# Kernel tuning notes

Measured on AMD Instinct MI355X. Metric: run time of the kernel, lower is better.

The kernel has to match this reference:

```python
import jax, jax.numpy as jnp
import numpy as np

D = 512
H = 8
HD = D // H
EPS = 1e-5
NEG_INF = -1e30


def _ln(x, g, b):
    mu = jnp.mean(x, axis=-1, keepdims=True)
    var = jnp.mean(jnp.square(x - mu), axis=-1, keepdims=True)
    return (x - mu) * jax.lax.rsqrt(var + EPS) * g + b


def setup_inputs() -> dict:
    key = jax.random.key(0)
    ks = jax.random.split(key, 8)
    V, M, S = 128, 128, 514  # seq includes 2 head tokens (cls+dist)
    inp = {
        "video_embeds": jax.random.normal(ks[0], (V, D), jnp.float32),
        "music_features": jax.random.normal(ks[1], (M, S, D), jnp.float32),
        "music_masks": jnp.ones((M, S - 2), jnp.int32),
    }
    wk = jax.random.split(ks[2], 5)
    for name, k in zip(["Wq", "Wk", "Wv", "Wo", "Wl"], wk):
        inp[name] = jax.random.normal(k, (D, D), jnp.float32) * 0.02
    for name in ["bq", "bk", "bv", "bo", "bl"]:
        inp[name] = jnp.zeros((D,), jnp.float32)
    for name in ["g1", "g2", "g3"]:
        inp[name] = jnp.ones((D,), jnp.float32)
    for name in ["b1", "b2", "b3"]:
        inp[name] = jnp.zeros((D,), jnp.float32)
    return inp


def reference(video_embeds, music_features, music_masks,
              Wq, bq, Wk, bk, Wv, bv, Wo, bo, Wl, bl,
              g1, b1, g2, b2, g3, b3):
    # drop cls + dist tokens
    mf = music_features[:, 2:, :]  # (M, f, D)
    ve = _ln(video_embeds, g1, b1)  # (V, D)
    mf = _ln(mf, g1, b1)
    V = ve.shape[0]
    M, f, _ = mf.shape

    q = (ve @ Wq.T + bq).reshape(V, H, HD).transpose(1, 0, 2)        # (H, V, hd)
    k = (mf @ Wk.T + bk).reshape(M, f, H, HD).transpose(0, 2, 1, 3)  # (M, H, f, hd)
    v = (mf @ Wv.T + bv).reshape(M, f, H, HD).transpose(0, 2, 1, 3)  # (M, H, f, hd)

    logits = jnp.einsum('hvd,mhfd->vmhf', q, k) / np.sqrt(HD).astype(np.float32)
    mask = music_masks[None, :, None, :]  # (1, M, 1, f)
    logits = jnp.where(mask == 0, NEG_INF, logits)
    w = jax.nn.softmax(logits, axis=-1)
    attn = jnp.einsum('vmhf,mhfd->vmhd', w, v).reshape(V, M, D)
    attn = attn @ Wo.T + bo

    attn = _ln(attn, g2, b2)
    out = attn + (attn @ Wl.T + bl)  # dropout = identity in eval
    return _ln(out, g3, b3)
```

## Files before the change

### kernel.cpp

```cpp
#include <hip/hip_runtime.h>
#include <hip/hip_bf16.h>

typedef unsigned int uint;
typedef unsigned short ushort;
typedef __bf16 bf16;
typedef bf16 bf16x8 __attribute__((ext_vector_type(8)));
typedef float f32x4 __attribute__((ext_vector_type(4)));
typedef ushort ushort4v __attribute__((ext_vector_type(4)));

__device__ __forceinline__ float bf2f(ushort u) {
  union { uint u; float f; } v; v.u = ((uint)u) << 16; return v.f;
}
__device__ __forceinline__ ushort f2bf(float f) {
  union { float f; uint u; } v; v.f = f;
  uint u = v.u;
  uint r = (u + 0x7fffu + ((u >> 16) & 1u)) >> 16;
  return (ushort)r;
}

__device__ __forceinline__ void gl2lds16(const void* g, void* l) {
  __builtin_amdgcn_global_load_lds(
      (const __attribute__((address_space(1))) void*)g,
      (__attribute__((address_space(3))) void*)l, 16, 0, 0);
}

__device__ __forceinline__ void ln_rows(
    int mode, int nrows, int blk, int nblk, int tid,
    const void* __restrict__ srcA, const void* __restrict__ srcB,
    const float* __restrict__ g, const float* __restrict__ b,
    void* __restrict__ dst)
{
  const int l = tid & 63;
  const int nw = nblk * 4;
  for (int row = blk * 4 + (tid >> 6); row < nrows; row += nw) {
    float x[8];
    if (mode <= 1) {
      const float* s;
      if (mode == 0) {
        s = (const float*)srcA + (size_t)row * 512;
      } else {
        int mm = row >> 9, fi = row & 511;
        s = (const float*)srcA + ((size_t)mm * 514 + 2 + fi) * 512;
      }
      float4 a0 = *(const float4*)(s + l * 4);
      float4 a1 = *(const float4*)(s + 256 + l * 4);
      x[0] = a0.x; x[1] = a0.y; x[2] = a0.z; x[3] = a0.w;
      x[4] = a1.x; x[5] = a1.y; x[6] = a1.z; x[7] = a1.w;
    } else if (mode == 2) {
      const ushort* s = (const ushort*)srcA + (size_t)row * 512;
      uint4 u = *(const uint4*)(s + l * 8);
      x[0] = bf2f((ushort)u.x); x[1] = bf2f((ushort)(u.x >> 16));
      x[2] = bf2f((ushort)u.y); x[3] = bf2f((ushort)(u.y >> 16));
      x[4] = bf2f((ushort)u.z); x[5] = bf2f((ushort)(u.z >> 16));
      x[6] = bf2f((ushort)u.w); x[7] = bf2f((ushort)(u.w >> 16));
    } else {
      const ushort* sa = (const ushort*)srcA + (size_t)row * 512;
      const ushort* sb = (const ushort*)srcB + (size_t)row * 512;
      uint4 ua = *(const uint4*)(sa + l * 8);
      uint4 ub = *(const uint4*)(sb + l * 8);
      x[0] = bf2f((ushort)ua.x) + bf2f((ushort)ub.x);
      x[1] = bf2f((ushort)(ua.x >> 16)) + bf2f((ushort)(ub.x >> 16));
      x[2] = bf2f((ushort)ua.y) + bf2f((ushort)ub.y);
      x[3] = bf2f((ushort)(ua.y >> 16)) + bf2f((ushort)(ub.y >> 16));
      x[4] = bf2f((ushort)ua.z) + bf2f((ushort)ub.z);
      x[5] = bf2f((ushort)(ua.z >> 16)) + bf2f((ushort)(ub.z >> 16));
      x[6] = bf2f((ushort)ua.w) + bf2f((ushort)ub.w);
      x[7] = bf2f((ushort)(ua.w >> 16)) + bf2f((ushort)(ub.w >> 16));
    }
    float sum = 0.f, sq = 0.f;
    #pragma unroll
    for (int j = 0; j < 8; ++j) { sum += x[j]; sq += x[j] * x[j]; }
    #pragma unroll
    for (int o = 1; o < 64; o <<= 1) {
      sum += __shfl_xor(sum, o);
      sq  += __shfl_xor(sq, o);
    }
    const float inv = 1.f / 512.f;
    float mu = sum * inv;
    float var = sq * inv - mu * mu;
    float rstd = rsqrtf(var + 1e-5f);

    float gv[8], bv[8];
    if (mode <= 1) {
      float4 g0 = *(const float4*)(g + l * 4);
      float4 g1 = *(const float4*)(g + 256 + l * 4);
      float4 b0 = *(const float4*)(b + l * 4);
      float4 b1 = *(const float4*)(b + 256 + l * 4);
      gv[0] = g0.x; gv[1] = g0.y; gv[2] = g0.z; gv[3] = g0.w;
      gv[4] = g1.x; gv[5] = g1.y; gv[6] = g1.z; gv[7] = g1.w;
      bv[0] = b0.x; bv[1] = b0.y; bv[2] = b0.z; bv[3] = b0.w;
      bv[4] = b1.x; bv[5] = b1.y; bv[6] = b1.z; bv[7] = b1.w;
    } else {
      float4 g0 = *(const float4*)(g + l * 8);
      float4 g1 = *(const float4*)(g + l * 8 + 4);
      float4 b0 = *(const float4*)(b + l * 8);
      float4 b1 = *(const float4*)(b + l * 8 + 4);
      gv[0] = g0.x; gv[1] = g0.y; gv[2] = g0.z; gv[3] = g0.w;
      gv[4] = g1.x; gv[5] = g1.y; gv[6] = g1.z; gv[7] = g1.w;
      bv[0] = b0.x; bv[1] = b0.y; bv[2] = b0.z; bv[3] = b0.w;
      bv[4] = b1.x; bv[5] = b1.y; bv[6] = b1.z; bv[7] = b1.w;
    }
    float y[8];
    #pragma unroll
    for (int j = 0; j < 8; ++j) y[j] = (x[j] - mu) * rstd * gv[j] + bv[j];

    if (mode <= 1) {
      ushort* d = (ushort*)dst + (size_t)row * 512;
      ushort4v p0, p1;
      #pragma unroll
      for (int j = 0; j < 4; ++j) { p0[j] = f2bf(y[j]); p1[j] = f2bf(y[4 + j]); }
      *(ushort4v*)(d + l * 4) = p0;
      *(ushort4v*)(d + 256 + l * 4) = p1;
    } else if (mode == 2) {
      ushort* d = (ushort*)dst + (size_t)row * 512;
      uint4 o;
      o.x = (uint)f2bf(y[0]) | ((uint)f2bf(y[1]) << 16);
      o.y = (uint)f2bf(y[2]) | ((uint)f2bf(y[3]) << 16);
      o.z = (uint)f2bf(y[4]) | ((uint)f2bf(y[5]) << 16);
      o.w = (uint)f2bf(y[6]) | ((uint)f2bf(y[7]) << 16);
      *(uint4*)(d + l * 8) = o;
    } else {
      float* d = (float*)dst + (size_t)row * 512;
      float4 o0, o1;
      o0.x = y[0]; o0.y = y[1]; o0.z = y[2]; o0.w = y[3];
      o1.x = y[4]; o1.y = y[5]; o1.z = y[6]; o1.w = y[7];
      *(float4*)(d + l * 8) = o0;
      *(float4*)(d + l * 8 + 4) = o1;
    }
  }
}

__global__ __launch_bounds__(256) void ln512v(
    int mode, int nrows,
    const void* __restrict__ srcA, const void* __restrict__ srcB,
    const float* __restrict__ g, const float* __restrict__ b,
    void* __restrict__ dst)
{
  ln_rows(mode, nrows, blockIdx.x, gridDim.x, threadIdx.x, srcA, srcB, g, b, dst);
}

struct PreArgs {
  const float* s0; const float* s1; const float* s2; const float* s3; const float* s4;
  ushort* d0; ushort* d1; ushort* d2; ushort* d3; ushort* d4;
  const float* video; const float* music;
  const float* g1; const float* b1;
  ushort* veln; ushort* mfln;
};
__global__ __launch_bounds__(256) void preamble(PreArgs a) {
  int bb = blockIdx.x;
  if (bb < 640) {
    int t = bb * 256 + threadIdx.x;
    int which = t >> 15;
    int e = (t & 32767) * 8;
    const float* s = which == 0 ? a.s0 : which == 1 ? a.s1 : which == 2 ? a.s2 : which == 3 ? a.s3 : a.s4;
    ushort*      d = which == 0 ? a.d0 : which == 1 ? a.d1 : which == 2 ? a.d2 : which == 3 ? a.d3 : a.d4;
    float4 v0 = *(const float4*)(s + e);
    float4 v1 = *(const float4*)(s + e + 4);
    uint4 o;
    o.x = (uint)f2bf(v0.x) | ((uint)f2bf(v0.y) << 16);
    o.y = (uint)f2bf(v0.z) | ((uint)f2bf(v0.w) << 16);
    o.z = (uint)f2bf(v1.x) | ((uint)f2bf(v1.y) << 16);
    o.w = (uint)f2bf(v1.z) | ((uint)f2bf(v1.w) << 16);
    *(uint4*)(d + e) = o;
  } else if (bb < 672) {
    ln_rows(0, 128, bb - 640, 32, threadIdx.x, a.video, nullptr, a.g1, a.b1, a.veln);
  } else {
    ln_rows(1, 65536, bb - 672, 2048, threadIdx.x, a.music, nullptr, a.g1, a.b1, a.mfln);
  }
}

__global__ __launch_bounds__(256) void gemm_t3(
    const ushort* __restrict__ A, const ushort* __restrict__ W,
    const float* __restrict__ bias, ushort* __restrict__ C,
    float scale, int vt_mode)
{
  __shared__ __align__(16) ushort As[2][128 * 64];
  __shared__ __align__(16) ushort Bs[2][128 * 64];
  const int tid = threadIdx.x;
  const int w = tid >> 6, l = tid & 63;
  const int lg = l >> 4, lr = l & 15;
  const int wr = w >> 1, wc = w & 1;

  int nwg = gridDim.x * gridDim.y;
  int bid = blockIdx.y * gridDim.x + blockIdx.x;
  if ((nwg & 7) == 0) bid = (bid & 7) * (nwg >> 3) + (bid >> 3);
  const int bx = bid % gridDim.x, by = bid / gridDim.x;
  const int row0 = by * 128, col0 = bx * 128;

  f32x4 acc[4][4];
  #pragma unroll
  for (int i = 0; i < 4; i++)
    #pragma unroll
    for (int j = 0; j < 4; j++) { f32x4 z = {0.f,0.f,0.f,0.f}; acc[i][j] = z; }

  size_t asrc[4], wsrc[4]; int ldst[4];
  #pragma unroll
  for (int c2 = 0; c2 < 4; ++c2) {
    int c = c2 * 256 + tid;
    int r = c >> 3, j = c & 7;
    int koff = (j ^ (r & 7)) * 8;
    asrc[c2] = (size_t)(row0 + r) * 512 + koff;
    wsrc[c2] = (size_t)(col0 + r) * 512 + koff;
    ldst[c2] = (c2 * 256 + w * 64) * 8;
  }

  auto stage = [&](int pb, int kk) {
    #pragma unroll
    for (int c2 = 0; c2 < 4; ++c2) {
      gl2lds16(A + asrc[c2] + kk * 64, &As[pb][ldst[c2]]);
      gl2lds16(W + wsrc[c2] + kk * 64, &Bs[pb][ldst[c2]]);
    }
  };
  auto compute = [&](int pb) {
    #pragma unroll
    for (int ks = 0; ks < 2; ++ks) {
      bf16x8 af[4], bfr[4];
      #pragma unroll
      for (int mi = 0; mi < 4; ++mi) {
        int r = wr * 64 + mi * 16 + lr;
        af[mi] = *(const bf16x8*)(&As[pb][r * 64 + ((ks * 32 + lg * 8) ^ ((r & 7) * 8))]);
      }
      #pragma unroll
      for (int ni = 0; ni < 4; ++ni) {
        int r = wc * 64 + ni * 16 + lr;
        bfr[ni] = *(const bf16x8*)(&Bs[pb][r * 64 + ((ks * 32 + lg * 8) ^ ((r & 7) * 8))]);
      }
      #pragma unroll
      for (int mi = 0; mi < 4; ++mi)
        #pragma unroll
        for (int ni = 0; ni < 4; ++ni)
          acc[mi][ni] = __builtin_amdgcn_mfma_f32_16x16x32_bf16(af[mi], bfr[ni], acc[mi][ni], 0, 0, 0);
    }
  };

  stage(0, 0);
  __syncthreads();
  int cur = 0;
  #pragma unroll
  for (int kk = 0; kk < 7; ++kk) {
    stage(cur ^ 1, kk + 1);
    compute(cur);
    __syncthreads();
    cur ^= 1;
  }
  compute(cur);

  #pragma unroll
  for (int ni = 0; ni < 4; ++ni) {
    int cg = col0 + wc * 64 + ni * 16 + lr;
    float bc = bias[cg];
    #pragma unroll
    for (int mi = 0; mi < 4; ++mi) {
      int rg0 = row0 + wr * 64 + mi * 16 + lg * 4;
      if (!vt_mode) {
        #pragma unroll
        for (int e = 0; e < 4; ++e) {
          float v = (acc[mi][ni][e] + bc) * scale;
          C[(size_t)(rg0 + e) * 512 + cg] = f2bf(v);
        }
      } else {
        int m = rg0 >> 9, fi = rg0 & 511;
        ushort4v pk;
        #pragma unroll
        for (int e = 0; e < 4; ++e) pk[e] = f2bf((acc[mi][ni][e] + bc) * scale);
        *(ushort4v*)(C + (size_t)(m * 512 + cg) * 512 + fi) = pk;
      }
    }
  }
}

__global__ __launch_bounds__(256) void attn_kernel(
    const ushort* __restrict__ q, const ushort* __restrict__ k,
    const ushort* __restrict__ vt, const int* __restrict__ masks,
    ushort* __restrict__ attn)
{
  __shared__ __align__(16) ushort Qs[128 * 64];
  __shared__ __align__(16) ushort Ks[64 * 64];
  __shared__ __align__(16) ushort Vs[64 * 64];
  __shared__ __align__(16) ushort Ps[4][32 * 64];
  __shared__ float maskf[64];
  __shared__ float stats[4][32];

  const int tid = threadIdx.x;
  const int w = tid >> 6, l = tid & 63;
  const int lg = l >> 4, lr = l & 15;
  const int m = blockIdx.x >> 3, h = blockIdx.x & 7;

  const size_t kbase = (size_t)(m * 512) * 512 + h * 64;
  const size_t vbase = (size_t)(m * 512 + h * 64) * 512;

  #pragma unroll
  for (int c2 = 0; c2 < 4; ++c2) {
    int c = c2 * 256 + tid;
    int r = c >> 3, j = c & 7;
    gl2lds16(q + (size_t)r * 512 + h * 64 + ((j * 8) ^ ((r & 7) * 8)),
             Qs + (c2 * 256 + w * 64) * 8);
  }

  f32x4 acc[2][4];
  #pragma unroll
  for (int i = 0; i < 2; i++)
    #pragma unroll
    for (int j = 0; j < 4; j++) { f32x4 z = {0.f,0.f,0.f,0.f}; acc[i][j] = z; }
  float m_run[2] = {-INFINITY, -INFINITY};
  float l_run[2] = {0.f, 0.f};
  bf16x8 qf[2][2];

  for (int it = 0; it < 8; ++it) {
    const int f0 = it * 64;
    #pragma unroll
    for (int c2 = 0; c2 < 2; ++c2) {
      int c = c2 * 256 + tid;
      int r = c >> 3, j = c & 7;
      int off = (j * 8) ^ ((r & 7) * 8);
      gl2lds16(k + kbase + (size_t)(f0 + r) * 512 + off, Ks + (c2 * 256 + w * 64) * 8);
      gl2lds16(vt + vbase + (size_t)r * 512 + f0 + off, Vs + (c2 * 256 + w * 64) * 8);
    }
    if (tid < 64) maskf[tid] = masks[m * 512 + f0 + tid] ? 0.f : -1e30f;
    __syncthreads();

    if (it == 0) {
      #pragma unroll
      for (int nv = 0; nv < 2; ++nv)
        #pragma unroll
        for (int k2 = 0; k2 < 2; ++k2) {
          int v = w * 32 + nv * 16 + lr;
          qf[nv][k2] = *(const bf16x8*)(Qs + v * 64 + ((k2 * 32 + lg * 8) ^ ((v & 7) * 8)));
        }
    }

    f32x4 s[4][2];
    #pragma unroll
    for (int mi = 0; mi < 4; mi++)
      #pragma unroll
      for (int nv = 0; nv < 2; nv++) { f32x4 z = {0.f,0.f,0.f,0.f}; s[mi][nv] = z; }
    #pragma unroll
    for (int k2 = 0; k2 < 2; ++k2) {
      bf16x8 kf[4];
      #pragma unroll
      for (int mi = 0; mi < 4; ++mi) {
        int f = mi * 16 + lr;
        kf[mi] = *(const bf16x8*)(Ks + f * 64 + ((k2 * 32 + lg * 8) ^ ((f & 7) * 8)));
      }
      __builtin_amdgcn_s_setprio(1);
      #pragma unroll
      for (int mi = 0; mi < 4; ++mi)
        #pragma unroll
        for (int nv = 0; nv < 2; ++nv)
          s[mi][nv] = __builtin_amdgcn_mfma_f32_16x16x32_bf16(kf[mi], qf[nv][k2], s[mi][nv], 0, 0, 0);
      __builtin_amdgcn_s_setprio(0);
    }

    float mk[4][4];
    #pragma unroll
    for (int mi = 0; mi < 4; mi++)
      #pragma unroll
      for (int e = 0; e < 4; e++) mk[mi][e] = maskf[mi * 16 + lg * 4 + e];

    #pragma unroll
    for (int nv = 0; nv < 2; ++nv) {
      float cmax = -INFINITY;
      #pragma unroll
      for (int mi = 0; mi < 4; mi++)
        #pragma unroll
        for (int e = 0; e < 4; e++) {
          s[mi][nv][e] += mk[mi][e];
          cmax = fmaxf(cmax, s[mi][nv][e]);
        }
      cmax = fmaxf(cmax, __shfl_xor(cmax, 16));
      cmax = fmaxf(cmax, __shfl_xor(cmax, 32));
      float mnew = fmaxf(m_run[nv], cmax);
      float sc = __expf(m_run[nv] - mnew);
      float csum = 0.f;
      int vloc = nv * 16 + lr;
      #pragma unroll
      for (int mi = 0; mi < 4; mi++) {
        ushort4v pk;
        #pragma unroll
        for (int e = 0; e < 4; e++) {
          float p = __expf(s[mi][nv][e] - mnew);
          csum += p;
          pk[e] = f2bf(p);
        }
        int f = mi * 16 + lg * 4;
        *(ushort4v*)(&Ps[w][vloc * 64 + (f ^ ((vloc & 7) * 8))]) = pk;
      }
      csum += __shfl_xor(csum, 16);
      csum += __shfl_xor(csum, 32);
      l_run[nv] = l_run[nv] * sc + csum;
      m_run[nv] = mnew;
      if (lg == 0) stats[w][vloc] = sc;
    }

    #pragma unroll
    for (int mi2 = 0; mi2 < 2; ++mi2)
      #pragma unroll
      for (int e = 0; e < 4; ++e) {
        float sc = stats[w][mi2 * 16 + lg * 4 + e];
        #pragma unroll
        for (int nd = 0; nd < 4; ++nd) acc[mi2][nd][e] *= sc;
      }

    #pragma unroll
    for (int k2 = 0; k2 < 2; ++k2) {
      bf16x8 pf[2], vf[4];
      #pragma unroll
      for (int mi2 = 0; mi2 < 2; ++mi2) {
        int vloc = mi2 * 16 + lr;
        pf[mi2] = *(const bf16x8*)(&Ps[w][vloc * 64 + ((k2 * 32 + lg * 8) ^ ((vloc & 7) * 8))]);
      }
      #pragma unroll
      for (int nd = 0; nd < 4; ++nd) {
        int d = nd * 16 + lr;
        vf[nd] = *(const bf16x8*)(Vs + d * 64 + ((k2 * 32 + lg * 8) ^ ((d & 7) * 8)));
      }
      __builtin_amdgcn_s_setprio(1);
      #pragma unroll
      for (int mi2 = 0; mi2 < 2; ++mi2)
        #pragma unroll
        for (int nd = 0; nd < 4; ++nd)
          acc[mi2][nd] = __builtin_amdgcn_mfma_f32_16x16x32_bf16(pf[mi2], vf[nd], acc[mi2][nd], 0, 0, 0);
      __builtin_amdgcn_s_setprio(0);
    }
    __syncthreads();
  }

  #pragma unroll
  for (int nv = 0; nv < 2; ++nv)
    if (lg == 0) stats[w][nv * 16 + lr] = 1.f / l_run[nv];
  #pragma unroll
  for (int mi2 = 0; mi2 < 2; ++mi2)
    #pragma unroll
    for (int e = 0; e < 4; ++e) {
      float invl = stats[w][mi2 * 16 + lg * 4 + e];
      int vg = w * 32 + mi2 * 16 + lg * 4 + e;
      #pragma unroll
      for (int nd = 0; nd < 4; ++nd) {
        int d = nd * 16 + lr;
        attn[(size_t)(vg * 128 + m) * 512 + h * 64 + d] = f2bf(acc[mi2][nd][e] * invl);
      }
    }
}

extern "C" void kernel_launch(void* const* d_in, const int* in_sizes, int n_in,
                              void* d_out, int out_size, void* d_ws, size_t ws_size,
                              hipStream_t stream) {
  const float* video = (const float*)d_in[0];
  const float* music = (const float*)d_in[1];
  const int*   masks = (const int*)d_in[2];
  const float* Wq = (const float*)d_in[3];
  const float* Wk = (const float*)d_in[4];
  const float* Wv = (const float*)d_in[5];
  const float* Wo = (const float*)d_in[6];
  const float* Wl = (const float*)d_in[7];
  const float* bq = (const float*)d_in[8];
  const float* bk = (const float*)d_in[9];
  const float* bv = (const float*)d_in[10];
  const float* bo = (const float*)d_in[11];
  const float* bl = (const float*)d_in[12];
  const float* g1 = (const float*)d_in[13];
  const float* g2 = (const float*)d_in[14];
  const float* g3 = (const float*)d_in[15];
  const float* b1 = (const float*)d_in[16];
  const float* b2 = (const float*)d_in[17];
  const float* b3 = (const float*)d_in[18];

  char* ws = (char*)d_ws;
  ushort* mfln = (ushort*)(ws);
  ushort* kbuf = (ushort*)(ws + 67108864);
  ushort* vtb  = (ushort*)(ws + 134217728);
  ushort* attn = (ushort*)(ws + 201326592);
  ushort* c1   = (ushort*)(ws + 218103808);
  ushort* xbuf = (ushort*)(ws + 234881024);
  ushort* veln = (ushort*)(ws + 251658240);
  ushort* qbuf = (ushort*)(ws + 251789312);
  ushort* wqb  = (ushort*)(ws + 251920384);
  ushort* wkb  = wqb + 262144;
  ushort* wvb  = wkb + 262144;
  ushort* wob  = wvb + 262144;
  ushort* wlb  = wob + 262144;

  PreArgs pa = {Wq, Wk, Wv, Wo, Wl, wqb, wkb, wvb, wob, wlb,
                video, music, g1, b1, veln, mfln};
  preamble<<<2720, 256, 0, stream>>>(pa);

  gemm_t3<<<dim3(4, 1), 256, 0, stream>>>(veln, wqb, bq, qbuf, 0.125f, 0);
  gemm_t3<<<dim3(4, 512), 256, 0, stream>>>(mfln, wkb, bk, kbuf, 1.f, 0);
  gemm_t3<<<dim3(4, 512), 256, 0, stream>>>(mfln, wvb, bv, vtb, 1.f, 1);

  attn_kernel<<<1024, 256, 0, stream>>>(qbuf, kbuf, vtb, masks, attn);

  gemm_t3<<<dim3(4, 128), 256, 0, stream>>>(attn, wob, bo, c1, 1.f, 0);
  ln512v<<<2048, 256, 0, stream>>>(2, 16384, c1, nullptr, g2, b2, xbuf);
  gemm_t3<<<dim3(4, 128), 256, 0, stream>>>(xbuf, wlb, bl, c1, 1.f, 0);
  ln512v<<<2048, 256, 0, stream>>>(3, 16384, xbuf, c1, g3, b3, d_out);
}
```

Before: 282.3 us.

## Use 256x256-tile 8-wave GEMM with interleaved staging for K/V projections

```diff
diff --git a/kernel.cpp b/kernel.cpp
--- a/kernel.cpp
+++ b/kernel.cpp
@@ -169,6 +169,111 @@
   }
 }
 
+__global__ __launch_bounds__(512) void gemm8p(
+    const ushort* __restrict__ Ag, const ushort* __restrict__ Wg,
+    const float* __restrict__ bias, ushort* __restrict__ C,
+    float scale, int vt_mode)
+{
+  __shared__ __align__(16) ushort As[2][2][128 * 64];
+  __shared__ __align__(16) ushort Bs[2][2][128 * 64];
+  const int tid = threadIdx.x;
+  const int w = tid >> 6, l = tid & 63;
+  const int lg = l >> 4, lr = l & 15;
+  const int wr = w >> 2, wc = w & 3;
+  const int rr8 = tid >> 3;
+  const int jj = tid & 7;
+  const int kx = (jj ^ (rr8 & 7)) * 8;
+
+  int bid = blockIdx.y * gridDim.x + blockIdx.x;
+  int pair = bid >> 1, npair = (gridDim.x * gridDim.y) >> 1;
+  if ((npair & 7) == 0) pair = (pair & 7) * (npair >> 3) + (pair >> 3);
+  const int row0 = pair * 256;
+  const int col0 = (bid & 1) * 256;
+
+  f32x4 acc[8][4];
+  #pragma unroll
+  for (int i = 0; i < 8; i++)
+    #pragma unroll
+    for (int j = 0; j < 4; j++) { f32x4 z = {0.f,0.f,0.f,0.f}; acc[i][j] = z; }
+
+  auto stage = [&](int bi, int kt) {
+    int b4 = bi & 3;
+    int rt = b4 * 64 + rr8;
+    int rbase = b4 * 64 + w * 8;
+    int h = rbase >> 7;
+    int lofs = (rbase & 127) * 64;
+    if (bi < 4)
+      gl2lds16(Ag + (size_t)(row0 + rt) * 512 + kt * 64 + kx, &As[kt & 1][h][lofs]);
+    else
+      gl2lds16(Wg + (size_t)(col0 + rt) * 512 + kt * 64 + kx, &Bs[kt & 1][h][lofs]);
+  };
+
+  #pragma unroll
+  for (int bi = 0; bi < 8; ++bi) stage(bi, 0);
+
+  bf16x8 bfr[4][2];
+  for (int t = 0; t < 8; ++t) {
+    asm volatile("s_waitcnt vmcnt(0)" ::: "memory");
+    __builtin_amdgcn_s_barrier();
+    const int buf = t & 1;
+    #pragma unroll
+    for (int p = 0; p < 4; ++p) {
+      bf16x8 af[2][2];
+      #pragma unroll
+      for (int d = 0; d < 2; ++d) {
+        int ra = (2 * p + d) * 16 + lr;
+        #pragma unroll
+        for (int ks = 0; ks < 2; ++ks)
+          af[d][ks] = *(const bf16x8*)(&As[buf][wr][ra * 64 + ((ks * 32 + lg * 8) ^ ((ra & 7) * 8))]);
+      }
+      if (p == 0) {
+        #pragma unroll
+        for (int ni = 0; ni < 4; ++ni) {
+          int cb = wc * 64 + ni * 16 + lr;
+          int hb = cb >> 7, rb = cb & 127;
+          #pragma unroll
+          for (int ks = 0; ks < 2; ++ks)
+            bfr[ni][ks] = *(const bf16x8*)(&Bs[buf][hb][rb * 64 + ((ks * 32 + lg * 8) ^ ((rb & 7) * 8))]);
+        }
+      }
+      if (t < 7) { stage(2 * p, t + 1); stage(2 * p + 1, t + 1); }
+      __builtin_amdgcn_s_barrier();
+      __builtin_amdgcn_s_setprio(1);
+      #pragma unroll
+      for (int ks = 0; ks < 2; ++ks)
+        #pragma unroll
+        for (int d = 0; d < 2; ++d)
+          #pragma unroll
+          for (int ni = 0; ni < 4; ++ni)
+            acc[2 * p + d][ni] = __builtin_amdgcn_mfma_f32_16x16x32_bf16(
+                af[d][ks], bfr[ni][ks], acc[2 * p + d][ni], 0, 0, 0);
+      __builtin_amdgcn_s_setprio(0);
+      if (p < 3) __builtin_amdgcn_s_barrier();
+    }
+  }
+
+  #pragma unroll
+  for (int ni = 0; ni < 4; ++ni) {
+    int cg = col0 + wc * 64 + ni * 16 + lr;
+    float bc = bias[cg];
+    #pragma unroll
+    for (int mi = 0; mi < 8; ++mi) {
+      int rg0 = row0 + wr * 128 + mi * 16 + lg * 4;
+      if (!vt_mode) {
+        #pragma unroll
+        for (int e = 0; e < 4; ++e)
+          C[(size_t)(rg0 + e) * 512 + cg] = f2bf((acc[mi][ni][e] + bc) * scale);
+      } else {
+        int m = rg0 >> 9, fi = rg0 & 511;
+        ushort4v pk;
+        #pragma unroll
+        for (int e = 0; e < 4; ++e) pk[e] = f2bf((acc[mi][ni][e] + bc) * scale);
+        *(ushort4v*)(C + (size_t)(m * 512 + cg) * 512 + fi) = pk;
+      }
+    }
+  }
+}
+
 __global__ __launch_bounds__(256) void gemm_t3(
     const ushort* __restrict__ A, const ushort* __restrict__ W,
     const float* __restrict__ bias, ushort* __restrict__ C,
@@ -485,8 +590,8 @@
   preamble<<<2720, 256, 0, stream>>>(pa);
 
   gemm_t3<<<dim3(4, 1), 256, 0, stream>>>(veln, wqb, bq, qbuf, 0.125f, 0);
-  gemm_t3<<<dim3(4, 512), 256, 0, stream>>>(mfln, wkb, bk, kbuf, 1.f, 0);
-  gemm_t3<<<dim3(4, 512), 256, 0, stream>>>(mfln, wvb, bv, vtb, 1.f, 1);
+  gemm8p<<<dim3(2, 256), 512, 0, stream>>>(mfln, wkb, bk, kbuf, 1.f, 0);
+  gemm8p<<<dim3(2, 256), 512, 0, stream>>>(mfln, wvb, bv, vtb, 1.f, 1);
 
   attn_kernel<<<1024, 256, 0, stream>>>(qbuf, kbuf, vtb, masks, attn);
 
```

Result: slower. 295.6 us (+4.7%).
